# Kernel tuning notes

Measured on AMD Instinct MI355X. Metric: run time of the kernel, lower is better.

## Reference

```python
import jax, jax.numpy as jnp
import numpy as np
from jax import lax

OBJ = 224
K = 8
IMG_MEAN = np.array([0.485, 0.456, 0.406], np.float32)
IMG_STD = np.array([0.229, 0.224, 0.225], np.float32)
OFF9 = np.array([[-1,-1],[-1,0],[-1,1],[0,-1],[0,0],[0,1],[1,-1],[1,0],[1,1]], np.float32)


def setup_inputs() -> dict:
    key = jax.random.key(0)
    ks = jax.random.split(key, 16)
    B, N = 8, 2048
    s = 0.05
    return {
        'points':   jax.random.normal(ks[0], (B, N, 3), jnp.float32),
        'w_in':     jax.random.normal(ks[1], (8, 3)) * s,
        'b_in':     jax.random.normal(ks[2], (8,)) * s,
        'w_graph':  jax.random.normal(ks[3], (64, 16)) * s,
        'gn_g':     jnp.ones((64,), jnp.float32),
        'gn_b':     jnp.zeros((64,), jnp.float32),
        'w_proj':   jax.random.normal(ks[4], (64, 64)) * s,
        'b_proj':   jax.random.normal(ks[5], (64,)) * s,
        'bb_w1':    jax.random.normal(ks[6], (64, 64, 3, 3)) * s,
        'bb_g1':    jnp.ones((64,), jnp.float32),
        'bb_b1':    jnp.zeros((64,), jnp.float32),
        'bb_w2':    jax.random.normal(ks[7], (64, 64, 3, 3)) * s,
        'bb_g2':    jnp.ones((64,), jnp.float32),
        'bb_b2':    jnp.zeros((64,), jnp.float32),
        'w_blkout': jax.random.normal(ks[8], (64, 64)) * s,
        'b_blkout': jax.random.normal(ks[9], (64,)) * s,
        'w_img':    jax.random.normal(ks[10], (3, 64)) * s,
        'b_img':    jax.random.normal(ks[11], (3,)) * s,
    }


def _knn_idx(coor, k):
    # coor: [B,N,3] -> idx of k nearest neighbors (incl. self): [B,N,k]
    sq = jnp.sum(coor * coor, axis=-1)                       # [B,N]
    d = sq[:, :, None] + sq[:, None, :] - 2.0 * jnp.einsum('bnd,bmd->bnm', coor, coor)
    _, idx = lax.top_k(-d, k)
    return idx


def _conv3x3(x, w):
    return lax.conv_general_dilated(x, w, (1, 1), 'SAME',
                                    dimension_numbers=('NCHW', 'OIHW', 'NCHW'))


def reference(points, w_in, b_in, w_graph, gn_g, gn_b, w_proj, b_proj,
              bb_w1, bb_g1, bb_b1, bb_w2, bb_g2, bb_b2,
              w_blkout, b_blkout, w_img, b_img):
    pc = points
    B, N, _ = pc.shape
    # ---- grid index computation (proj2color) ----
    pc_min = jnp.min(pc, axis=1, keepdims=True)[:, :, :2]              # [B,1,2]
    pc_range = jnp.max(pc, axis=1) - jnp.min(pc, axis=1)               # [B,3]
    grid = jnp.max(pc_range[:, :2], axis=-1) / (OBJ - 3)               # [B]
    idx_xy = jnp.floor((pc[:, :, :2] - pc_min) / grid[:, None, None])  # [B,N,2]
    dense = (idx_xy[:, :, None, :] + jnp.asarray(OFF9)[None, None]).reshape(B, N * 9, 2) + 1.0
    center = jnp.floor((jnp.max(dense, 1) + jnp.min(dense, 1)) / 2.0).astype(jnp.int32).astype(jnp.float32)
    off = OBJ / 2 - center - 1.0                                       # [B,2]
    dense = dense + off[:, None, :]
    dense = dense + (dense < 0).astype(jnp.float32) - (dense > OBJ - 1).astype(jnp.float32)
    lin = (dense[:, :, 0] * OBJ + dense[:, :, 1]).astype(jnp.int32)    # [B,N*9]
    # ---- point feature path ----
    f0 = jnp.einsum('bnc,oc->bno', pc, w_in) + b_in                    # [B,N,8]
    idx = _knn_idx(pc, K)                                              # [B,N,K]
    fn = jax.vmap(lambda fb, ib: fb[ib])(f0, idx)                      # [B,N,K,8]
    feat = jnp.concatenate([fn - f0[:, :, None, :],
                            jnp.broadcast_to(f0[:, :, None, :], fn.shape)], axis=-1)  # [B,N,K,16]
    g = jnp.einsum('bnkc,oc->bnko', feat, w_graph)                     # [B,N,K,64]
    # GroupNorm(4, 64): normalize per-sample over (N, K, 16 channels/group)
    gg = g.reshape(B, N, K, 4, 16)
    mu = jnp.mean(gg, axis=(1, 2, 4), keepdims=True)
    var = jnp.var(gg, axis=(1, 2, 4), keepdims=True)
    g = ((gg - mu) / jnp.sqrt(var + 1e-5)).reshape(B, N, K, 64) * gn_g + gn_b
    g = jnp.where(g >= 0, g, 0.2 * g)                                  # LeakyReLU(0.2)
    g = jnp.max(g, axis=2)                                             # max over k: [B,N,64]
    f = jnp.einsum('bnc,oc->bno', g, w_proj) + b_proj                  # [B,N,64]
    f9 = jnp.broadcast_to(f[:, :, None, :], (B, N, 9, 64)).reshape(B, N * 9, 64)
    # ---- scatter-sum onto 224x224 grid ----
    seg = lin + jnp.arange(B, dtype=jnp.int32)[:, None] * (OBJ * OBJ)
    out = jax.ops.segment_sum(f9.reshape(-1, 64), seg.reshape(-1), num_segments=B * OBJ * OBJ)
    res = out.reshape(B, OBJ, OBJ, 64).transpose(0, 3, 1, 2)           # [B,64,224,224]
    # ---- BasicBlock (eval-mode BN as scale/shift) + 1x1 convs ----
    h = _conv3x3(res, bb_w1) * bb_g1[None, :, None, None] + bb_b1[None, :, None, None]
    h = jax.nn.relu(h)
    h = _conv3x3(h, bb_w2) * bb_g2[None, :, None, None] + bb_b2[None, :, None, None]
    h = jax.nn.relu(h + res)
    h = jnp.einsum('bchw,oc->bohw', h, w_blkout) + b_blkout[None, :, None, None]
    img = jnp.einsum('bchw,oc->bohw', h, w_img) + b_img[None, :, None, None]
    img = jax.nn.sigmoid(img)
    mean = jnp.asarray(IMG_MEAN)[None, :, None, None]
    std = jnp.asarray(IMG_STD)[None, :, None, None]
    return (img - mean) / std
```

## Files before the change

kernel.cpp:

```cpp
#include <hip/hip_runtime.h>
#include <math.h>

#define BB 8
#define NN 2048
#define KNNK 8
#define SEG 8
#define SEGN (NN/SEG)
#define OBJ 224
#define HWD (OBJ*OBJ)

typedef _Float16 f16x8 __attribute__((ext_vector_type(8)));
typedef _Float16 f16x4 __attribute__((ext_vector_type(4)));
typedef float    f32x4v __attribute__((ext_vector_type(4)));

constexpr size_t RES_SZ  = (size_t)BB*HWD*64;
constexpr size_t F_SZ    = (size_t)BB*NN*64;
constexpr size_t F0_SZ   = (size_t)BB*NN*8;
constexpr size_t RES_OFF = 0;
constexpr size_t H1_OFF  = RES_SZ;
constexpr size_t F_OFF   = 2*RES_SZ;
constexpr size_t F0_OFF  = F_OFF + F_SZ;
constexpr size_t BP_OFF  = F0_OFF + F0_SZ;
constexpr size_t GS_OFF  = BP_OFF + 128;
constexpr size_t GM_OFF  = GS_OFF + 64;
constexpr size_t WT1_OFF = GM_OFF + 64;
constexpr size_t WTF_SZ  = 46080;
constexpr size_t WT2_OFF = WT1_OFF + WTF_SZ;
constexpr size_t INT_OFF = WT2_OFF + WTF_SZ;

__global__ void k0_wtf(const float* __restrict__ w, _Float16* __restrict__ wf) {
    int i = blockIdx.x*256 + threadIdx.x;
    if (i >= 92160) return;
    int kk = i % 40;
    int o  = (i/40) & 63;
    int hl = (i/2560) & 1;
    int kb = (i/5120) & 1;
    int tp = i/10240;
    _Float16 v = (_Float16)0.f;
    if (kk < 32) {
        int c = kb*32 + kk;
        float val = w[(size_t)(o*64 + c)*9 + tp];
        _Float16 hi = (_Float16)val;
        v = hl ? (_Float16)(val - (float)hi) : hi;
    }
    wf[i] = v;
}

__global__ void k1_params(const float* __restrict__ pc, float* __restrict__ bparam) {
    __shared__ float r0[256], r1[256], r2[256], r3[256];
    __shared__ float sh[4];
    int b = blockIdx.x, t = threadIdx.x;
    const float* p = pc + (size_t)b*NN*3;
    float mnx=1e30f, mxx=-1e30f, mny=1e30f, mxy=-1e30f;
    for (int n=t; n<NN; n+=256) {
        float x=p[3*n], y=p[3*n+1];
        mnx=fminf(mnx,x); mxx=fmaxf(mxx,x); mny=fminf(mny,y); mxy=fmaxf(mxy,y);
    }
    r0[t]=mnx; r1[t]=mxx; r2[t]=mny; r3[t]=mxy;
    __syncthreads();
    for (int s=128; s>0; s>>=1) {
        if (t<s) { r0[t]=fminf(r0[t],r0[t+s]); r1[t]=fmaxf(r1[t],r1[t+s]);
                   r2[t]=fminf(r2[t],r2[t+s]); r3[t]=fmaxf(r3[t],r3[t+s]); }
        __syncthreads();
    }
    if (t==0) {
        float rx = __fsub_rn(r1[0], r0[0]);
        float ry = __fsub_rn(r3[0], r2[0]);
        sh[0]=r0[0]; sh[1]=r2[0];
        float c221 = __fdiv_rn(1.0f, (float)(OBJ-3));
        float grid = __fmul_rn(fmaxf(rx,ry), c221);
        sh[2] = grid;
        sh[3] = __fdiv_rn(1.0f, grid);
    }
    __syncthreads();
    float minx=sh[0], miny=sh[1], rgrid=sh[3];
    mnx=1e30f; mxx=-1e30f; mny=1e30f; mxy=-1e30f;
    for (int n=t; n<NN; n+=256) {
        float ix = floorf(__fmul_rn(__fsub_rn(p[3*n],   minx), rgrid));
        float iy = floorf(__fmul_rn(__fsub_rn(p[3*n+1], miny), rgrid));
        mnx=fminf(mnx,ix); mxx=fmaxf(mxx,ix); mny=fminf(mny,iy); mxy=fmaxf(mxy,iy);
    }
    __syncthreads();
    r0[t]=mnx; r1[t]=mxx; r2[t]=mny; r3[t]=mxy;
    __syncthreads();
    for (int s=128; s>0; s>>=1) {
        if (t<s) { r0[t]=fminf(r0[t],r0[t+s]); r1[t]=fmaxf(r1[t],r1[t+s]);
                   r2[t]=fminf(r2[t],r2[t+s]); r3[t]=fmaxf(r3[t],r3[t+s]); }
        __syncthreads();
    }
    if (t==0) {
        float cx = floorf((r1[0] + 2.0f + r0[0]) * 0.5f);
        float cy = floorf((r3[0] + 2.0f + r2[0]) * 0.5f);
        bparam[b*8+0]=minx; bparam[b*8+1]=miny; bparam[b*8+2]=sh[3];
        bparam[b*8+3]=112.0f - cx - 1.0f;
        bparam[b*8+4]=112.0f - cy - 1.0f;
    }
}

__global__ void k2_lin(const float* __restrict__ pc, const float* __restrict__ bparam,
                       int* __restrict__ lin) {
    int i = blockIdx.x*256 + threadIdx.x;
    if (i >= BB*NN) return;
    int b = i / NN;
    float x = pc[(size_t)i*3], y = pc[(size_t)i*3+1];
    float minx=bparam[b*8], miny=bparam[b*8+1], rgrid=bparam[b*8+2];
    float offx=bparam[b*8+3], offy=bparam[b*8+4];
    float ix = floorf(__fmul_rn(__fsub_rn(x, minx), rgrid));
    float iy = floorf(__fmul_rn(__fsub_rn(y, miny), rgrid));
    const float o9x[9] = {-1,-1,-1, 0,0,0, 1,1,1};
    const float o9y[9] = {-1, 0, 1,-1,0,1,-1,0,1};
#pragma unroll
    for (int j=0; j<9; ++j) {
        float dx = ix + o9x[j] + 1.0f + offx;
        float dy = iy + o9y[j] + 1.0f + offy;
        dx += (dx < 0.f ? 1.f : 0.f) - (dx > 223.f ? 1.f : 0.f);
        dy += (dy < 0.f ? 1.f : 0.f) - (dy > 223.f ? 1.f : 0.f);
        lin[(size_t)i*9 + j] = (int)(dx*224.f + dy);
    }
}

__global__ void k3_f0(const float* __restrict__ pc, const float* __restrict__ w_in,
                      const float* __restrict__ b_in, float* __restrict__ f0) {
    int i = blockIdx.x*256 + threadIdx.x;
    if (i >= BB*NN*8) return;
    int o = i & 7; int bn = i >> 3;
    float x=pc[(size_t)bn*3], y=pc[(size_t)bn*3+1], z=pc[(size_t)bn*3+2];
    f0[i] = x*w_in[o*3] + y*w_in[o*3+1] + z*w_in[o*3+2] + b_in[o];
}

__global__ __launch_bounds__(256) void k4_knn(const float* __restrict__ pc,
                                              float* __restrict__ pd,
                                              int* __restrict__ pi) {
    __shared__ float4 pts[SEGN];
    int b = blockIdx.y, t = threadIdx.x, seg = blockIdx.z;
    const float* p = pc + (size_t)b*NN*3;
    int m0 = seg*SEGN;
    for (int m=t; m<SEGN; m+=256) {
        int mm = m0 + m;
        float x=p[3*mm], y=p[3*mm+1], z=p[3*mm+2];
        float sq = __fadd_rn(__fadd_rn(__fmul_rn(x,x), __fmul_rn(y,y)), __fmul_rn(z,z));
        pts[m] = make_float4(x, y, z, sq);
    }
    __syncthreads();
    int n = blockIdx.x*256 + t;
    float mx = p[3*n], my = p[3*n+1], mz = p[3*n+2];
    float msq = __fadd_rn(__fadd_rn(__fmul_rn(mx,mx), __fmul_rn(my,my)), __fmul_rn(mz,mz));
    float bd[KNNK]; int bi[KNNK];
#pragma unroll
    for (int j=0; j<KNNK; ++j) { bd[j]=1e30f; bi[j]=0; }
#pragma unroll 8
    for (int m=0; m<SEGN; ++m) {
        float4 q = pts[m];
        float dot = __fadd_rn(__fadd_rn(__fmul_rn(mz,q.z), __fmul_rn(my,q.y)),
                              __fmul_rn(mx,q.x));
        float d = __fsub_rn(__fadd_rn(msq, q.w), __fmul_rn(2.0f, dot));
        if (d < bd[KNNK-1]) {
            float v=d; int vi=m0+m;
#pragma unroll
            for (int j=0; j<KNNK; ++j) {
                if (v < bd[j]) { float tv=bd[j]; int ti=bi[j]; bd[j]=v; bi[j]=vi; v=tv; vi=ti; }
            }
        }
    }
    size_t base = (((size_t)b*NN + n)*SEG + seg)*KNNK;
#pragma unroll
    for (int j=0; j<KNNK; ++j) { pd[base+j] = bd[j]; pi[base+j] = bi[j]; }
}

__global__ void k4b_merge(const float* __restrict__ pd, const int* __restrict__ pi,
                          int* __restrict__ nidx) {
    int i = blockIdx.x*256 + threadIdx.x;
    if (i >= BB*NN) return;
    size_t base = (size_t)i*SEG*KNNK;
    float bd[KNNK]; int bi[KNNK];
#pragma unroll
    for (int j=0; j<KNNK; ++j) { bd[j]=1e30f; bi[j]=0x7fffffff; }
#pragma unroll
    for (int s=0; s<SEG; ++s) {
#pragma unroll
        for (int j=0; j<KNNK; ++j) {
            float v = pd[base + s*KNNK + j];
            int  vi = pi[base + s*KNNK + j];
            if (v < bd[KNNK-1]) {
                float cv=v; int ci=vi;
#pragma unroll
                for (int q=0; q<KNNK; ++q) {
                    if (cv < bd[q]) { float tv=bd[q]; int ti=bi[q]; bd[q]=cv; bi[q]=ci; cv=tv; ci=ti; }
                }
            }
        }
    }
#pragma unroll
    for (int j=0; j<KNNK; ++j) nidx[(size_t)i*KNNK + j] = bi[j];
}

__device__ __forceinline__ void build_feat(int t, int b, int n0,
        const float* __restrict__ f0, const int* __restrict__ nidx,
        float feat[4][8][16]) {
    int pt = t >> 6, k = (t >> 3) & 7, c = t & 7;
    int n  = n0 + pt;
    int nb = nidx[((size_t)b*NN + n)*8 + k];
    float f0c = f0[((size_t)b*NN + n)*8 + c];
    float fnc = f0[((size_t)b*NN + nb)*8 + c];
    feat[pt][k][c]   = fnc - f0c;
    feat[pt][k][c+8] = f0c;
}

__global__ __launch_bounds__(256) void k5_stats(const float* __restrict__ f0,
        const int* __restrict__ nidx, const float* __restrict__ w_graph,
        float* __restrict__ gsum) {
    __shared__ float wgT[16*64];
    __shared__ float feat[4][8][16];
    __shared__ float part[4][4][2];
    int t = threadIdx.x;
    for (int i=t; i<1024; i+=256) wgT[(i&15)*64 + (i>>4)] = w_graph[i];
    int blk = blockIdx.x;
    int b = blk >> 9, n0 = (blk & 511)*4;
    build_feat(t, b, n0, f0, nidx, feat);
    __syncthreads();
    int pt = t >> 6, o = t & 63;
    float s = 0.f, s2 = 0.f;
#pragma unroll
    for (int k=0; k<8; ++k) {
        float g = 0.f;
#pragma unroll
        for (int c=0; c<16; ++c) g = fmaf(feat[pt][k][c], wgT[c*64+o], g);
        s += g; s2 += g*g;
    }
#pragma unroll
    for (int off=8; off; off>>=1) {
        s  += __shfl_down(s,  off, 16);
        s2 += __shfl_down(s2, off, 16);
    }
    if ((o & 15) == 0) { part[pt][o>>4][0] = s; part[pt][o>>4][1] = s2; }
    __syncthreads();
    if (t < 8) {
        int grp = t >> 1, which = t & 1;
        float v = part[0][grp][which] + part[1][grp][which]
                + part[2][grp][which] + part[3][grp][which];
        atomicAdd(&gsum[(b*4+grp)*2 + which], v);
    }
}

__global__ void k5b_finalize(const float* __restrict__ gsum, float* __restrict__ gmu) {
    int t = threadIdx.x;
    if (t < 32) {
        const float cnt = (float)(NN*KNNK*16);
        float mu = gsum[t*2] / cnt;
        float var = gsum[t*2+1] / cnt - mu*mu;
        gmu[t*2]   = mu;
        gmu[t*2+1] = 1.0f / sqrtf(var + 1e-5f);
    }
}

__global__ __launch_bounds__(256) void k6_point(const float* __restrict__ f0,
        const int* __restrict__ nidx, const float* __restrict__ w_graph,
        const float* __restrict__ gmu, const float* __restrict__ gn_g,
        const float* __restrict__ gn_b, const float* __restrict__ w_proj,
        const float* __restrict__ b_proj, float* __restrict__ f) {
    __shared__ float wgT[16*64];
    __shared__ float wpT[64*64];
    __shared__ float feat[4][8][16];
    __shared__ float gmax_s[4][64];
    int t = threadIdx.x;
    for (int i=t; i<1024; i+=256) wgT[(i&15)*64 + (i>>4)] = w_graph[i];
    for (int i=t; i<4096; i+=256) wpT[(i&63)*64 + (i>>6)] = w_proj[i];
    int blk = blockIdx.x;
    int b = blk >> 9, n0 = (blk & 511)*4;
    build_feat(t, b, n0, f0, nidx, feat);
    __syncthreads();
    int pt = t >> 6, o = t & 63;
    int grp = o >> 4;
    float mu = gmu[(b*4+grp)*2], rsig = gmu[(b*4+grp)*2+1];
    float ga = gn_g[o], be = gn_b[o];
    float gm = -1e30f;
#pragma unroll
    for (int k=0; k<8; ++k) {
        float g = 0.f;
#pragma unroll
        for (int c=0; c<16; ++c) g = fmaf(feat[pt][k][c], wgT[c*64+o], g);
        float v = (g - mu)*rsig*ga + be;
        v = (v >= 0.f) ? v : 0.2f*v;
        gm = fmaxf(gm, v);
    }
    gmax_s[pt][o] = gm;
    __syncthreads();
    float acc = b_proj[o];
#pragma unroll
    for (int c=0; c<64; ++c) acc = fmaf(gmax_s[pt][c], wpT[c*64+o], acc);
    f[((size_t)b*NN + n0 + pt)*64 + o] = acc;
}

__global__ __launch_bounds__(256) void k7_scatter(const float* __restrict__ f,
        const int* __restrict__ lin, float* __restrict__ res) {
    int blk = blockIdx.x, t = threadIdx.x;
    int b = blk >> 9;
    int n = (blk & 511)*4 + (t >> 6);
    int o = t & 63;
    size_t bn = (size_t)b*NN + n;
    float v = f[bn*64 + o];
#pragma unroll
    for (int j=0; j<9; ++j) {
        int cell = lin[bn*9 + j];
        if (cell >= 0 && cell < HWD)
            atomicAdd(&res[((size_t)b*HWD + cell)*64 + o], v);
    }
}

#define LDS4_BYTES 51840

#define MFMA16(A,B,C) __builtin_amdgcn_mfma_f32_16x16x32_f16(A,B,C,0,0,0)

#define LOADW(TP, H0, L0, H1, L1) { \
    const _Float16* wb_ = wf + (size_t)((TP)*10240) + obase; \
    H0 = *(const f16x8*)wb_;          L0 = *(const f16x8*)(wb_ + 2560); \
    H1 = *(const f16x8*)(wb_ + 5120); L1 = *(const f16x8*)(wb_ + 7680); }

#define TAPC(TP, H0, L0, H1, L1) { \
    _Pragma("unroll") \
    for (int m = 0; m < 8; ++m) { \
        int off_ = ((m + (TP)/3)*18 + lr + (TP)%3)*72 + lg*8; \
        f16x8 ah0 = *(const f16x8*)&haloH[off_]; \
        f16x8 al0 = *(const f16x8*)&haloL[off_]; \
        acc[m] = MFMA16(ah0, H0, acc[m]); \
        acc[m] = MFMA16(al0, H0, acc[m]); \
        acc[m] = MFMA16(ah0, L0, acc[m]); \
        f16x8 ah1 = *(const f16x8*)&haloH[off_ + 32]; \
        f16x8 al1 = *(const f16x8*)&haloL[off_ + 32]; \
        acc[m] = MFMA16(ah1, H1, acc[m]); \
        acc[m] = MFMA16(al1, H1, acc[m]); \
        acc[m] = MFMA16(ah1, L1, acc[m]); \
    } }

__device__ __forceinline__ void conv_mfma_body(
        const float* __restrict__ sp, const _Float16* __restrict__ wf,
        _Float16* haloH, _Float16* haloL,
        int x0, int y0, int t, int wid, int lr, int lg, f32x4v acc[8]) {
    float4 vreg[12];
#pragma unroll
    for (int j = 0; j < 12; ++j) {
        int i = j*256 + t; if (i > 2879) i = 2879;
        int cell = i >> 4, c4 = i & 15;
        int gy = y0 - 1 + cell/18, gx = x0 - 1 + cell%18;
        int cy = gy < 0 ? 0 : (gy > OBJ-1 ? OBJ-1 : gy);
        int cx = gx < 0 ? 0 : (gx > OBJ-1 ? OBJ-1 : gx);
        vreg[j] = *(const float4*)(sp + ((size_t)cy*OBJ + cx)*64 + c4*4);
    }
#pragma unroll
    for (int j = 0; j < 12; ++j) {
        int i = j*256 + t;
        if (i <= 2879) {
            int cell = i >> 4, c4 = i & 15;
            int gy = y0 - 1 + cell/18, gx = x0 - 1 + cell%18;
            bool inb = ((unsigned)gy < (unsigned)OBJ) && ((unsigned)gx < (unsigned)OBJ);
            float4 v = vreg[j];
            if (!inb) v = make_float4(0.f,0.f,0.f,0.f);
            _Float16 a0=(_Float16)v.x, a1=(_Float16)v.y, a2=(_Float16)v.z, a3=(_Float16)v.w;
            f16x4 hv = {a0, a1, a2, a3};
            f16x4 lv = {(_Float16)(v.x-(float)a0), (_Float16)(v.y-(float)a1),
                        (_Float16)(v.z-(float)a2), (_Float16)(v.w-(float)a3)};
            *(f16x4*)&haloH[cell*72 + c4*4] = hv;
            *(f16x4*)&haloL[cell*72 + c4*4] = lv;
        }
    }
    const int obase = (16*wid + lr)*40 + lg*8;
    f16x8 whA0, wlA0, whA1, wlA1, whB0, wlB0, whB1, wlB1;
    LOADW(0, whA0, wlA0, whA1, wlA1);
    LOADW(1, whB0, wlB0, whB1, wlB1);
    __syncthreads();
    TAPC(0, whA0, wlA0, whA1, wlA1);  LOADW(2, whA0, wlA0, whA1, wlA1);
    TAPC(1, whB0, wlB0, whB1, wlB1);  LOADW(3, whB0, wlB0, whB1, wlB1);
    TAPC(2, whA0, wlA0, whA1, wlA1);  LOADW(4, whA0, wlA0, whA1, wlA1);
    TAPC(3, whB0, wlB0, whB1, wlB1);  LOADW(5, whB0, wlB0, whB1, wlB1);
    TAPC(4, whA0, wlA0, whA1, wlA1);  LOADW(6, whA0, wlA0, whA1, wlA1);
    TAPC(5, whB0, wlB0, whB1, wlB1);  LOADW(7, whB0, wlB0, whB1, wlB1);
    TAPC(6, whA0, wlA0, whA1, wlA1);  LOADW(8, whA0, wlA0, whA1, wlA1);
    TAPC(7, whB0, wlB0, whB1, wlB1);
    TAPC(8, whA0, wlA0, whA1, wlA1);
}

__global__ __launch_bounds__(256, 1) void k8m_conv1(
        const float* __restrict__ src, const _Float16* __restrict__ wf,
        const float* __restrict__ g1, const float* __restrict__ b1,
        float* __restrict__ dst) {
    __shared__ __align__(16) char smem[LDS4_BYTES];
    _Float16* haloH = (_Float16*)smem;
    _Float16* haloL = (_Float16*)(smem + 25920);
    int flat = blockIdx.x + 14*(blockIdx.y + 28*blockIdx.z);
    int b = flat & 7, rem = flat >> 3;
    int by = rem/14, bx = rem - by*14;
    int x0 = bx*16, y0 = by*8;
    int t = threadIdx.x, wid = t >> 6, lr = t & 15, lg = (t >> 4) & 3;
    f32x4v acc[8];
#pragma unroll
    for (int m=0;m<8;++m) acc[m] = (f32x4v){0.f,0.f,0.f,0.f};
    conv_mfma_body(src + (size_t)b*HWD*64, wf, haloH, haloL,
                   x0, y0, t, wid, lr, lg, acc);
    float gv = g1[16*wid+lr], bv = b1[16*wid+lr];
    float* dp = dst + (size_t)b*HWD*64;
#pragma unroll
    for (int m = 0; m < 8; ++m) {
        size_t rowb = ((size_t)(y0+m)*OBJ + x0)*64 + 16*wid + lr;
#pragma unroll
        for (int r = 0; r < 4; ++r) {
            int px = lg*4 + r;
            dp[rowb + (size_t)px*64] = fmaxf(fmaf(acc[m][r], gv, bv), 0.f);
        }
    }
}

__global__ __launch_bounds__(256, 1) void k9m_conv2(
        const float* __restrict__ h1, const _Float16* __restrict__ wf,
        const float* __restrict__ g2, const float* __restrict__ b2,
        const float* __restrict__ resi,
        const float* __restrict__ wbk, const float* __restrict__ bbk,
        const float* __restrict__ wim, const float* __restrict__ bim,
        float* __restrict__ outp) {
    __shared__ __align__(16) char smem[LDS4_BYTES];
    _Float16* haloH = (_Float16*)smem;
    _Float16* haloL = (_Float16*)(smem + 25920);
    int flat = blockIdx.x + 14*(blockIdx.y + 28*blockIdx.z);
    int b = flat & 7, rem = flat >> 3;
    int by = rem/14, bx = rem - by*14;
    int x0 = bx*16, y0 = by*8;
    int t = threadIdx.x, wid = t >> 6, lr = t & 15, lg = (t >> 4) & 3;
    f32x4v acc[8];
#pragma unroll
    for (int m=0;m<8;++m) acc[m] = (f32x4v){0.f,0.f,0.f,0.f};
    conv_mfma_body(h1 + (size_t)b*HWD*64, wf, haloH, haloL,
                   x0, y0, t, wid, lr, lg, acc);
    f16x8 wbh0, wbl0, wbh1, wbl1;
#define LOADWBK(KB, H, L) { \
    const float* wp_ = wbk + (size_t)(16*wid+lr)*64 + (KB)*32 + lg*8; \
    float4 w0_ = *(const float4*)wp_; \
    float4 w1_ = *(const float4*)(wp_+4); \
    const float* we_ = (const float*)&w0_; \
    const float* wo_ = (const float*)&w1_; \
    _Float16 h_[8]; _Float16 l_[8]; \
    _Pragma("unroll") \
    for (int e=0;e<4;++e) { h_[e]=(_Float16)we_[e]; l_[e]=(_Float16)(we_[e]-(float)h_[e]); } \
    _Pragma("unroll") \
    for (int e=0;e<4;++e) { h_[4+e]=(_Float16)wo_[e]; l_[4+e]=(_Float16)(wo_[e]-(float)h_[4+e]); } \
    H = (f16x8){h_[0],h_[1],h_[2],h_[3],h_[4],h_[5],h_[6],h_[7]}; \
    L = (f16x8){l_[0],l_[1],l_[2],l_[3],l_[4],l_[5],l_[6],l_[7]}; }
    LOADWBK(0, wbh0, wbl0);
    LOADWBK(1, wbh1, wbl1);
#undef LOADWBK
    float rv[8][4];
    {
        const float* rp = resi + (size_t)b*HWD*64 + 16*wid + lr;
#pragma unroll
        for (int m = 0; m < 8; ++m)
#pragma unroll
        for (int r = 0; r < 4; ++r)
            rv[m][r] = rp[((size_t)(y0+m)*OBJ + x0 + lg*4 + r)*64];
    }
    float g2v = g2[16*wid+lr], b2v = b2[16*wid+lr];
    __syncthreads();
    _Float16* thlH = (_Float16*)smem;
    _Float16* thlL = (_Float16*)(smem + 18432);
#pragma unroll
    for (int m = 0; m < 8; ++m)
#pragma unroll
    for (int r = 0; r < 4; ++r) {
        int pix = m*16 + lg*4 + r;
        float tv = fmaxf(fmaf(acc[m][r], g2v, b2v) + rv[m][r], 0.f);
        _Float16 hi = (_Float16)tv;
        thlH[pix*72 + 16*wid + lr] = hi;
        thlL[pix*72 + 16*wid + lr] = (_Float16)(tv - (float)hi);
    }
    __syncthreads();
    f32x4v a2[8];
#pragma unroll
    for (int m=0;m<8;++m) a2[m] = (f32x4v){0.f,0.f,0.f,0.f};
#pragma unroll
    for (int m = 0; m < 8; ++m) {
        int off0 = (m*16 + lr)*72 + lg*8;
        f16x8 ah0 = *(const f16x8*)&thlH[off0];
        f16x8 al0 = *(const f16x8*)&thlL[off0];
        a2[m] = MFMA16(ah0, wbh0, a2[m]);
        a2[m] = MFMA16(al0, wbh0, a2[m]);
        a2[m] = MFMA16(ah0, wbl0, a2[m]);
        f16x8 ah1 = *(const f16x8*)&thlH[off0 + 32];
        f16x8 al1 = *(const f16x8*)&thlL[off0 + 32];
        a2[m] = MFMA16(ah1, wbh1, a2[m]);
        a2[m] = MFMA16(al1, wbh1, a2[m]);
        a2[m] = MFMA16(ah1, wbl1, a2[m]);
    }
    __syncthreads();
    float* ureg = (float*)smem;
    float bkv = bbk[16*wid+lr];
#pragma unroll
    for (int m = 0; m < 8; ++m)
#pragma unroll
    for (int r = 0; r < 4; ++r) {
        int pix = m*16 + lg*4 + r;
        ureg[pix*67 + 16*wid + lr] = a2[m][r] + bkv;
    }
    __syncthreads();
    if (t < 128) {
        const float MEAN[3] = {0.485f, 0.456f, 0.406f};
        const float STDV[3] = {0.229f, 0.224f, 0.225f};
        int pix = t, py = pix >> 4, px = pix & 15;
#pragma unroll
        for (int o3 = 0; o3 < 3; ++o3) {
            float s = bim[o3];
            for (int c = 0; c < 64; ++c)
                s = fmaf(wim[o3*64 + c], ureg[pix*67 + c], s);
            float sig = 1.f/(1.f + expf(-s));
            outp[((size_t)(b*3 + o3))*HWD + (size_t)(y0+py)*OBJ + (x0+px)] =
                (sig - MEAN[o3]) / STDV[o3];
        }
    }
}

extern "C" void kernel_launch(void* const* d_in, const int* in_sizes, int n_in,
                              void* d_out, int out_size, void* d_ws, size_t ws_size,
                              hipStream_t stream) {
    const float* pc      = (const float*)d_in[0];
    const float* w_in    = (const float*)d_in[1];
    const float* b_in    = (const float*)d_in[2];
    const float* w_graph = (const float*)d_in[3];
    const float* gn_g    = (const float*)d_in[4];
    const float* gn_b    = (const float*)d_in[5];
    const float* w_proj  = (const float*)d_in[6];
    const float* b_proj  = (const float*)d_in[7];
    const float* bb_w1   = (const float*)d_in[8];
    const float* bb_g1   = (const float*)d_in[9];
    const float* bb_b1   = (const float*)d_in[10];
    const float* bb_w2   = (const float*)d_in[11];
    const float* bb_g2   = (const float*)d_in[12];
    const float* bb_b2   = (const float*)d_in[13];
    const float* w_blkout= (const float*)d_in[14];
    const float* b_blkout= (const float*)d_in[15];
    const float* w_img   = (const float*)d_in[16];
    const float* b_img   = (const float*)d_in[17];

    float* ws     = (float*)d_ws;
    float* res    = ws + RES_OFF;
    float* h1     = ws + H1_OFF;
    float* pd     = ws + H1_OFF;
    int*   pi     = (int*)(ws + H1_OFF + (size_t)BB*NN*SEG*KNNK);
    float* f      = ws + F_OFF;
    float* f0     = ws + F0_OFF;
    float* bparam = ws + BP_OFF;
    float* gsum   = ws + GS_OFF;
    float* gmu    = ws + GM_OFF;
    _Float16* wt1f = (_Float16*)(ws + WT1_OFF);
    _Float16* wt2f = (_Float16*)(ws + WT2_OFF);
    int*   lin    = (int*)(ws + INT_OFF);
    int*   nidx   = lin + (size_t)BB*NN*9;
    float* out    = (float*)d_out;

    hipMemsetAsync(res, 0, RES_SZ*sizeof(float), stream);
    hipMemsetAsync(gsum, 0, 64*sizeof(float), stream);

    k0_wtf<<<360, 256, 0, stream>>>(bb_w1, wt1f);
    k0_wtf<<<360, 256, 0, stream>>>(bb_w2, wt2f);
    k1_params<<<BB, 256, 0, stream>>>(pc, bparam);
    k2_lin<<<(BB*NN)/256, 256, 0, stream>>>(pc, bparam, lin);
    k3_f0<<<(BB*NN*8)/256, 256, 0, stream>>>(pc, w_in, b_in, f0);
    k4_knn<<<dim3(NN/256, BB, SEG), 256, 0, stream>>>(pc, pd, pi);
    k4b_merge<<<(BB*NN)/256, 256, 0, stream>>>(pd, pi, nidx);
    k5_stats<<<(BB*NN)/4, 256, 0, stream>>>(f0, nidx, w_graph, gsum);
    k5b_finalize<<<1, 64, 0, stream>>>(gsum, gmu);
    k6_point<<<(BB*NN)/4, 256, 0, stream>>>(f0, nidx, w_graph, gmu, gn_g, gn_b,
                                            w_proj, b_proj, f);
    k7_scatter<<<(BB*NN)/4, 256, 0, stream>>>(f, lin, res);
    k8m_conv1<<<dim3(14, 28, BB), 256, 0, stream>>>(res, wt1f, bb_g1, bb_b1, h1);
    k9m_conv2<<<dim3(14, 28, BB), 256, 0, stream>>>(h1, wt2f, bb_g2, bb_b2, res,
                                                    w_blkout, b_blkout, w_img, b_img, out);
}
```

Before: 652.0 us.

## Restructure 3x3 MFMA conv loop to reuse halo row loads across taps

The conv body now loads all nine taps' split-fp16 weights into registers up front and iterates over the ten halo rows. Each row's three dx-shifted A fragments are read from LDS once and reused for every output row they feed, instead of being reloaded per tap. This cuts LDS read traffic by about a factor of three. It costs many more live VGPRs (144 weight registers' worth of f16x8), which the launch_bounds(256,1) setting may absorb, with some risk of spills.

Result: faster. 554.1 us (-15.0%).

```diff
diff --git a/kernel.cpp b/kernel.cpp
--- a/kernel.cpp
+++ b/kernel.cpp
@@ -311,25 +311,29 @@
 
 #define MFMA16(A,B,C) __builtin_amdgcn_mfma_f32_16x16x32_f16(A,B,C,0,0,0)
 
-#define LOADW(TP, H0, L0, H1, L1) { \
-    const _Float16* wb_ = wf + (size_t)((TP)*10240) + obase; \
-    H0 = *(const f16x8*)wb_;          L0 = *(const f16x8*)(wb_ + 2560); \
-    H1 = *(const f16x8*)(wb_ + 5120); L1 = *(const f16x8*)(wb_ + 7680); }
-
-#define TAPC(TP, H0, L0, H1, L1) { \
+#define ROWC(R) { \
+    f16x8 ah0[3], al0[3], ah1[3], al1[3]; \
     _Pragma("unroll") \
-    for (int m = 0; m < 8; ++m) { \
-        int off_ = ((m + (TP)/3)*18 + lr + (TP)%3)*72 + lg*8; \
-        f16x8 ah0 = *(const f16x8*)&haloH[off_]; \
-        f16x8 al0 = *(const f16x8*)&haloL[off_]; \
-        acc[m] = MFMA16(ah0, H0, acc[m]); \
-        acc[m] = MFMA16(al0, H0, acc[m]); \
-        acc[m] = MFMA16(ah0, L0, acc[m]); \
-        f16x8 ah1 = *(const f16x8*)&haloH[off_ + 32]; \
-        f16x8 al1 = *(const f16x8*)&haloL[off_ + 32]; \
-        acc[m] = MFMA16(ah1, H1, acc[m]); \
-        acc[m] = MFMA16(al1, H1, acc[m]); \
-        acc[m] = MFMA16(ah1, L1, acc[m]); \
+    for (int dx = 0; dx < 3; ++dx) { \
+        int off_ = ((R)*18 + lr + dx)*72 + lg*8; \
+        ah0[dx] = *(const f16x8*)&haloH[off_]; \
+        al0[dx] = *(const f16x8*)&haloL[off_]; \
+        ah1[dx] = *(const f16x8*)&haloH[off_ + 32]; \
+        al1[dx] = *(const f16x8*)&haloL[off_ + 32]; \
+    } \
+    _Pragma("unroll") \
+    for (int dy = 0; dy < 3; ++dy) { \
+        if ((R) - dy >= 0 && (R) - dy <= 7) { \
+            _Pragma("unroll") \
+            for (int dx = 0; dx < 3; ++dx) { \
+                acc[(R)-dy] = MFMA16(ah0[dx], wh0[dy*3+dx], acc[(R)-dy]); \
+                acc[(R)-dy] = MFMA16(al0[dx], wh0[dy*3+dx], acc[(R)-dy]); \
+                acc[(R)-dy] = MFMA16(ah0[dx], wl0[dy*3+dx], acc[(R)-dy]); \
+                acc[(R)-dy] = MFMA16(ah1[dx], wh1[dy*3+dx], acc[(R)-dy]); \
+                acc[(R)-dy] = MFMA16(al1[dx], wh1[dy*3+dx], acc[(R)-dy]); \
+                acc[(R)-dy] = MFMA16(ah1[dx], wl1[dy*3+dx], acc[(R)-dy]); \
+            } \
+        } \
     } }
 
 __device__ __forceinline__ void conv_mfma_body(
@@ -364,19 +368,18 @@
         }
     }
     const int obase = (16*wid + lr)*40 + lg*8;
-    f16x8 whA0, wlA0, whA1, wlA1, whB0, wlB0, whB1, wlB1;
-    LOADW(0, whA0, wlA0, whA1, wlA1);
-    LOADW(1, whB0, wlB0, whB1, wlB1);
-    __syncthreads();
-    TAPC(0, whA0, wlA0, whA1, wlA1);  LOADW(2, whA0, wlA0, whA1, wlA1);
-    TAPC(1, whB0, wlB0, whB1, wlB1);  LOADW(3, whB0, wlB0, whB1, wlB1);
-    TAPC(2, whA0, wlA0, whA1, wlA1);  LOADW(4, whA0, wlA0, whA1, wlA1);
-    TAPC(3, whB0, wlB0, whB1, wlB1);  LOADW(5, whB0, wlB0, whB1, wlB1);
-    TAPC(4, whA0, wlA0, whA1, wlA1);  LOADW(6, whA0, wlA0, whA1, wlA1);
-    TAPC(5, whB0, wlB0, whB1, wlB1);  LOADW(7, whB0, wlB0, whB1, wlB1);
-    TAPC(6, whA0, wlA0, whA1, wlA1);  LOADW(8, whA0, wlA0, whA1, wlA1);
-    TAPC(7, whB0, wlB0, whB1, wlB1);
-    TAPC(8, whA0, wlA0, whA1, wlA1);
+    f16x8 wh0[9], wl0[9], wh1[9], wl1[9];
+#pragma unroll
+    for (int tp = 0; tp < 9; ++tp) {
+        const _Float16* wb_ = wf + (size_t)(tp*10240) + obase;
+        wh0[tp] = *(const f16x8*)wb_;
+        wl0[tp] = *(const f16x8*)(wb_ + 2560);
+        wh1[tp] = *(const f16x8*)(wb_ + 5120);
+        wl1[tp] = *(const f16x8*)(wb_ + 7680);
+    }
+    __syncthreads();
+    ROWC(0) ROWC(1) ROWC(2) ROWC(3) ROWC(4)
+    ROWC(5) ROWC(6) ROWC(7) ROWC(8) ROWC(9)
 }
 
 __global__ __launch_bounds__(256, 1) void k8m_conv1(
```
